# Kernel optimization log

Hardware: AMD Instinct MI355X
Metric: run time of the kernel (lower is better)

## Reference

```python
import jax, jax.numpy as jnp
import numpy as np

N, E = 50000, 800000
D_IN, D_HID, D_OUT, K = 128, 64, 64, 3
SLOPE = 0.2


def _xavier(key, shape):
    fan_out, fan_in = shape[0], shape[-1]
    if len(shape) == 3:  # att param (1, heads, 2*out)
        fan_out, fan_in = shape[1], shape[2]
    a = jnp.sqrt(6.0 / (fan_in + fan_out)).astype(jnp.float32)
    return jax.random.uniform(key, shape, jnp.float32, -a, a)


def setup_inputs() -> dict:
    key = jax.random.key(0)
    ks = jax.random.split(key, 9)
    x = jax.random.normal(ks[0], (N, D_IN), jnp.float32)
    edge_index = jax.random.randint(ks[1], (2, E), 0, N, jnp.int64)
    return {
        "x": x,
        "edge_index": edge_index,
        "W1": _xavier(ks[2], (D_HID, D_IN)),        # lin weight layer 1
        "att1": _xavier(ks[3], (1, 1, 2 * D_HID)),
        "bias1": jnp.zeros((D_HID,), jnp.float32),
        "resW1": _xavier(ks[4], (D_HID, D_IN)),     # res_fc (128 != 64)
        "W2": _xavier(ks[5], (D_OUT, D_HID)),       # lin weight layer 2
        "att2": _xavier(ks[6], (1, 1, 2 * D_OUT)),
        "bias2": jnp.zeros((D_OUT,), jnp.float32),
    }


def _agdn_conv(x, src, dst, W, att, bias, resW, heads):
    n = x.shape[0]
    h0 = (x @ W.T).reshape(n, heads, -1)                      # [N, h, out]
    feats = [h0]
    f = h0
    for _ in range(K):  # K-hop scatter-add propagation
        f = jax.ops.segment_sum(f[src], dst, num_segments=n)  # [N, h, out]
        feats.append(f)
    stack = jnp.stack(feats, axis=2)                          # [N, h, K+1, out]
    cat = jnp.concatenate(
        [jnp.broadcast_to(h0[:, :, None, :], stack.shape), stack], axis=-1
    )                                                         # [N, h, K+1, 2*out]
    score = jax.nn.leaky_relu((cat * att).sum(-1), SLOPE)     # [N, h, K+1]
    attn = jax.nn.softmax(score, axis=2)[..., None]
    out = (stack * attn).sum(axis=2).reshape(n, -1)           # [N, h*out]
    res = (x @ resW.T) if resW is not None else h0.reshape(n, -1)
    return out + res + bias


def reference(x, edge_index, W1, att1, bias1, resW1, W2, att2, bias2):
    src, dst = edge_index[0], edge_index[1]
    h = _agdn_conv(x, src, dst, W1, att1, bias1, resW1, heads=1)
    h = jax.nn.elu(h)  # eval mode: dropout is identity
    out = _agdn_conv(h, src, dst, W2, att2, bias2, None, heads=1)
    return out
```

## Files before the change

kernel.cpp:

```cpp
#include <hip/hip_runtime.h>
#include <math.h>


#define EPB 4096
#define CAP 8192

typedef __attribute__((ext_vector_type(8))) short bf16x8;
typedef __attribute__((ext_vector_type(4))) float f32x4;
typedef __attribute__((ext_vector_type(2))) float f32x2;

__device__ __forceinline__ float bf2f(unsigned short u)
{
    unsigned int t = ((unsigned int)u) << 16;
    return __builtin_bit_cast(float, t);
}
__device__ __forceinline__ unsigned short f2bf(float f)
{
    unsigned int t = __builtin_bit_cast(unsigned int, f);
    t += 0x7FFFu + ((t >> 16) & 1u);
    return (unsigned short)(t >> 16);
}
__device__ __forceinline__ float bflo(unsigned int u)
{
    return __builtin_bit_cast(float, u << 16);
}
__device__ __forceinline__ float bfhi(unsigned int u)
{
    return __builtin_bit_cast(float, u & 0xFFFF0000u);
}
__device__ __forceinline__ f32x2 up2v(unsigned int u)
{
    f32x2 r;
    r.x = bflo(u);
    r.y = bfhi(u);
    return r;
}

__global__ __launch_bounds__(256)
void convert_w_kernel(const float* __restrict__ W1, const float* __restrict__ Wres,
                      const float* __restrict__ W2,
                      unsigned short* __restrict__ w1b, unsigned short* __restrict__ w2b)
{
    int i = blockIdx.x * 256 + threadIdx.x;
    if (i < 8192)       w1b[i] = f2bf(W1[i]);
    else if (i < 16384) w1b[i] = f2bf(Wres[i - 8192]);
    else if (i < 20480) w2b[i - 16384] = f2bf(W2[i - 16384]);
}

#define LD1 136
__global__ __launch_bounds__(256)
void gemm_l1_mfma(const float* __restrict__ x,
                  const unsigned short* __restrict__ w1b,
                  unsigned short* __restrict__ h0, float* __restrict__ res, int n)
{
    __shared__ unsigned short xs[64 * LD1];
    __shared__ unsigned short ws[128 * LD1];
    const int tid = threadIdx.x;
    const int n0 = blockIdx.x * 64;

    for (int i = tid; i < 128 * 16; i += 256) {
        int r = i >> 4, c8 = (i & 15) * 8;
        *(uint4*)&ws[r * LD1 + c8] = *(const uint4*)&w1b[r * 128 + c8];
    }
    for (int i = tid; i < 64 * 32; i += 256) {
        int r = i >> 5, c4 = (i & 31) * 4;
        int nn = n0 + r;
        float4 v = (nn < n) ? *(const float4*)&x[(size_t)nn * 128 + c4]
                            : make_float4(0.f, 0.f, 0.f, 0.f);
        uint2 o;
        o.x = (unsigned)f2bf(v.x) | ((unsigned)f2bf(v.y) << 16);
        o.y = (unsigned)f2bf(v.z) | ((unsigned)f2bf(v.w) << 16);
        *(uint2*)&xs[r * LD1 + c4] = o;
    }
    __syncthreads();

    const int wv = tid >> 6, l = tid & 63;
    const int lrow = l & 15, lk = l >> 4;
    f32x4 acc[8] = {};
    const unsigned short* ax = &xs[(wv * 16 + lrow) * LD1 + lk * 8];
    const unsigned short* bw = &ws[lrow * LD1 + lk * 8];

    #pragma unroll
    for (int s = 0; s < 4; ++s) {
        bf16x8 a = *(const bf16x8*)&ax[s * 32];
        #pragma unroll
        for (int t = 0; t < 8; ++t) {
            bf16x8 b = *(const bf16x8*)&bw[(size_t)t * 16 * LD1 + s * 32];
            acc[t] = __builtin_amdgcn_mfma_f32_16x16x32_bf16(a, b, acc[t], 0, 0, 0);
        }
    }

    #pragma unroll
    for (int t = 0; t < 8; ++t) {
        #pragma unroll
        for (int r = 0; r < 4; ++r) {
            int node = n0 + wv * 16 + lk * 4 + r;
            if (node < n) {
                if (t < 4) h0[(size_t)node * 64 + t * 16 + lrow] = f2bf(acc[t][r]);
                else       res[(size_t)node * 64 + (t - 4) * 16 + lrow] = acc[t][r];
            }
        }
    }
}

#define LD2 72
__global__ __launch_bounds__(256)
void gemm_l2_mfma(const float* __restrict__ h,
                  const unsigned short* __restrict__ w2b,
                  unsigned short* __restrict__ h0, int n)
{
    __shared__ unsigned short xs[64 * LD2];
    __shared__ unsigned short ws[64 * LD2];
    const int tid = threadIdx.x;
    const int n0 = blockIdx.x * 64;

    for (int i = tid; i < 64 * 8; i += 256) {
        int r = i >> 3, c8 = (i & 7) * 8;
        *(uint4*)&ws[r * LD2 + c8] = *(const uint4*)&w2b[r * 64 + c8];
    }
    for (int i = tid; i < 64 * 16; i += 256) {
        int r = i >> 4, c4 = (i & 15) * 4;
        int nn = n0 + r;
        float4 v = (nn < n) ? *(const float4*)&h[(size_t)nn * 64 + c4]
                            : make_float4(0.f, 0.f, 0.f, 0.f);
        uint2 o;
        o.x = (unsigned)f2bf(v.x) | ((unsigned)f2bf(v.y) << 16);
        o.y = (unsigned)f2bf(v.z) | ((unsigned)f2bf(v.w) << 16);
        *(uint2*)&xs[r * LD2 + c4] = o;
    }
    __syncthreads();

    const int wv = tid >> 6, l = tid & 63;
    const int lrow = l & 15, lk = l >> 4;
    f32x4 acc[4] = {};
    const unsigned short* ax = &xs[(wv * 16 + lrow) * LD2 + lk * 8];
    const unsigned short* bw = &ws[lrow * LD2 + lk * 8];

    #pragma unroll
    for (int s = 0; s < 2; ++s) {
        bf16x8 a = *(const bf16x8*)&ax[s * 32];
        #pragma unroll
        for (int t = 0; t < 4; ++t) {
            bf16x8 b = *(const bf16x8*)&bw[(size_t)t * 16 * LD2 + s * 32];
            acc[t] = __builtin_amdgcn_mfma_f32_16x16x32_bf16(a, b, acc[t], 0, 0, 0);
        }
    }

    #pragma unroll
    for (int t = 0; t < 4; ++t) {
        #pragma unroll
        for (int r = 0; r < 4; ++r) {
            int node = n0 + wv * 16 + lk * 4 + r;
            if (node < n)
                h0[(size_t)node * 64 + t * 16 + lrow] = f2bf(acc[t][r]);
        }
    }
}

__global__ __launch_bounds__(256)
void part_hist_kernel(const int* __restrict__ dst, int* __restrict__ table,
                      int E, int NB)
{
    __shared__ int h[256];
    h[threadIdx.x] = 0;
    __syncthreads();
    int base = blockIdx.x * EPB;
    for (int i = threadIdx.x; i < EPB; i += 256) {
        int e = base + i;
        if (e < E) atomicAdd(&h[((unsigned)dst[e]) >> 8], 1);
    }
    __syncthreads();
    table[threadIdx.x * NB + blockIdx.x] = h[threadIdx.x];
}

__global__ __launch_bounds__(256)
void scanA_kernel(const int* __restrict__ cnt, int* __restrict__ excl,
                  int* __restrict__ bsum, int n)
{
    __shared__ int sh[256];
    int i = blockIdx.x * 256 + threadIdx.x;
    int v = (i < n) ? cnt[i] : 0;
    sh[threadIdx.x] = v;
    __syncthreads();
    #pragma unroll
    for (int off = 1; off < 256; off <<= 1) {
        int t = (threadIdx.x >= off) ? sh[threadIdx.x - off] : 0;
        __syncthreads();
        sh[threadIdx.x] += t;
        __syncthreads();
    }
    if (i < n) excl[i] = sh[threadIdx.x] - v;
    if (threadIdx.x == 255) bsum[blockIdx.x] = sh[255];
}

__global__ __launch_bounds__(256)
void scanB_kernel(const int* __restrict__ bsum, int* __restrict__ bofs, int nb)
{
    __shared__ int sh[256];
    int v = (threadIdx.x < nb) ? bsum[threadIdx.x] : 0;
    sh[threadIdx.x] = v;
    __syncthreads();
    #pragma unroll
    for (int off = 1; off < 256; off <<= 1) {
        int t = (threadIdx.x >= off) ? sh[threadIdx.x - off] : 0;
        __syncthreads();
        sh[threadIdx.x] += t;
        __syncthreads();
    }
    if (threadIdx.x < nb) bofs[threadIdx.x] = sh[threadIdx.x] - v;
}

__global__ __launch_bounds__(256)
void part_scatter_kernel(const int* __restrict__ src, const int* __restrict__ dst,
                         const int* __restrict__ exclT, const int* __restrict__ bofsT,
                         unsigned int* __restrict__ packed, int E, int NB)
{
    __shared__ int lhist[256];
    __shared__ int sh[256];
    __shared__ int lexcl[256];
    __shared__ int lcur[256];
    __shared__ int gb2[256];
    __shared__ unsigned int lp[EPB];
    __shared__ unsigned char lbin[EPB];

    const int tid = threadIdx.x;
    const int base = blockIdx.x * EPB;
    const int cntE = min(EPB, E - base);

    unsigned int pv[16];
    int pb[16];
    lhist[tid] = 0;
    __syncthreads();
    #pragma unroll
    for (int it = 0; it < 16; ++it) {
        int i = it * 256 + tid;
        pv[it] = 0; pb[it] = -1;
        if (i < cntE) {
            int e = base + i;
            unsigned int p = (((unsigned)dst[e]) << 16) | (unsigned)src[e];
            pv[it] = p;
            pb[it] = (int)(p >> 24);
            atomicAdd(&lhist[pb[it]], 1);
        }
    }
    __syncthreads();
    sh[tid] = lhist[tid];
    __syncthreads();
    #pragma unroll
    for (int off = 1; off < 256; off <<= 1) {
        int t = (tid >= off) ? sh[tid - off] : 0;
        __syncthreads();
        sh[tid] += t;
        __syncthreads();
    }
    lexcl[tid] = sh[tid] - lhist[tid];
    lcur[tid] = sh[tid] - lhist[tid];
    int ti = tid * NB + blockIdx.x;
    gb2[tid] = exclT[ti] + bofsT[ti >> 8] - lexcl[tid];
    __syncthreads();
    #pragma unroll
    for (int it = 0; it < 16; ++it) {
        if (pb[it] >= 0) {
            int slot = atomicAdd(&lcur[pb[it]], 1);
            lp[slot] = pv[it];
            lbin[slot] = (unsigned char)pb[it];
        }
    }
    __syncthreads();
    for (int i = tid; i < cntE; i += 256)
        packed[gb2[lbin[i]] + i] = lp[i];
}

__global__ __launch_bounds__(256)
void bucket_build_kernel(const unsigned int* __restrict__ packed,
                         const int* __restrict__ exclT, const int* __restrict__ bofsT,
                         int* __restrict__ rowptr, int* __restrict__ col,
                         int E, int NB, int N)
{
    __shared__ int h[256];
    __shared__ int sh[256];
    __shared__ int lcur[256];
    __shared__ int colL[CAP];

    const int b = blockIdx.x;
    const int t = threadIdx.x;
    int i0 = exclT[b * NB] + bofsT[(b * NB) >> 8];
    int bn = (b + 1) * NB;
    int i1 = exclT[bn] + bofsT[bn >> 8];

    h[t] = 0;
    __syncthreads();
    for (int i = i0 + t; i < i1; i += 256)
        atomicAdd(&h[(packed[i] >> 16) & 255], 1);
    __syncthreads();
    sh[t] = h[t];
    __syncthreads();
    #pragma unroll
    for (int off = 1; off < 256; off <<= 1) {
        int v = (t >= off) ? sh[t - off] : 0;
        __syncthreads();
        sh[t] += v;
        __syncthreads();
    }
    int excl = sh[t] - h[t];
    int d = b * 256 + t;
    if (d < N) rowptr[d] = i0 + excl;
    if (b == gridDim.x - 1 && t == 0) rowptr[N] = E;
    lcur[t] = excl;
    __syncthreads();
    for (int i = i0 + t; i < i1; i += 256) {
        unsigned int p = packed[i];
        int lo = (p >> 16) & 255;
        int s = (int)(p & 0xFFFFu);
        int r = atomicAdd(&lcur[lo], 1);
        if (r < CAP) colL[r] = s;
        else col[i0 + r] = s;
    }
    __syncthreads();
    int cB = i1 - i0;
    for (int i = t; i < cB && i < CAP; i += 256)
        col[i0 + i] = colL[i];
}

__global__ __launch_bounds__(256)
void hop_csr_kernel(const unsigned short* __restrict__ fin,
                    unsigned short* __restrict__ fout,
                    const int* __restrict__ rowptr, const int* __restrict__ col, int n)
{
    int node = blockIdx.x * 4 + (threadIdx.x >> 6);
    if (node >= n) return;
    int lane = threadIdx.x & 63;
    int sub = lane >> 3;
    int fo = (lane & 7) * 8;

    int beg = rowptr[node], end = rowptr[node + 1];
    int deg = end - beg;
    f32x2 ac[4] = {};
    for (int b = 0; b < deg; b += 16) {
        int e0 = beg + b + sub, e1 = e0 + 8;
        uint4 u0 = make_uint4(0, 0, 0, 0), u1 = make_uint4(0, 0, 0, 0);
        if (e0 < end) { int s = col[e0]; u0 = *(const uint4*)&fin[(size_t)s * 64 + fo]; }
        if (e1 < end) { int s = col[e1]; u1 = *(const uint4*)&fin[(size_t)s * 64 + fo]; }
        ac[0] += up2v(u0.x); ac[1] += up2v(u0.y);
        ac[2] += up2v(u0.z); ac[3] += up2v(u0.w);
        ac[0] += up2v(u1.x); ac[1] += up2v(u1.y);
        ac[2] += up2v(u1.z); ac[3] += up2v(u1.w);
    }
    float a[8] = {ac[0].x, ac[0].y, ac[1].x, ac[1].y,
                  ac[2].x, ac[2].y, ac[3].x, ac[3].y};
    #pragma unroll
    for (int off = 8; off <= 32; off <<= 1)
        #pragma unroll
        for (int k = 0; k < 8; ++k)
            a[k] += __shfl_xor(a[k], off);
    if (sub == 0) {
        uint4 o;
        o.x = (unsigned)f2bf(a[0]) | ((unsigned)f2bf(a[1]) << 16);
        o.y = (unsigned)f2bf(a[2]) | ((unsigned)f2bf(a[3]) << 16);
        o.z = (unsigned)f2bf(a[4]) | ((unsigned)f2bf(a[5]) << 16);
        o.w = (unsigned)f2bf(a[6]) | ((unsigned)f2bf(a[7]) << 16);
        *(uint4*)&fout[(size_t)node * 64 + fo] = o;
    }
}

template<int MODE>
__global__ __launch_bounds__(256)
void hop3_combine_kernel(const unsigned short* __restrict__ h0,
                         const unsigned short* __restrict__ f1,
                         const unsigned short* __restrict__ f2,
                         const float* __restrict__ res, const float* __restrict__ att,
                         const float* __restrict__ bias, float* __restrict__ out,
                         const int* __restrict__ rowptr, const int* __restrict__ col, int n)
{
    int node = blockIdx.x * 4 + (threadIdx.x >> 6);
    if (node >= n) return;
    int lane = threadIdx.x & 63;
    int sub = lane >> 3;
    int fo = (lane & 7) * 8;
    size_t rbase = (size_t)node * 64 + fo;

    int beg = rowptr[node], end = rowptr[node + 1];
    int deg = end - beg;
    f32x2 ac[4] = {};
    for (int b = 0; b < deg; b += 16) {
        int e0 = beg + b + sub, e1 = e0 + 8;
        uint4 u0 = make_uint4(0, 0, 0, 0), u1 = make_uint4(0, 0, 0, 0);
        if (e0 < end) { int s = col[e0]; u0 = *(const uint4*)&f2[(size_t)s * 64 + fo]; }
        if (e1 < end) { int s = col[e1]; u1 = *(const uint4*)&f2[(size_t)s * 64 + fo]; }
        ac[0] += up2v(u0.x); ac[1] += up2v(u0.y);
        ac[2] += up2v(u0.z); ac[3] += up2v(u0.w);
        ac[0] += up2v(u1.x); ac[1] += up2v(u1.y);
        ac[2] += up2v(u1.z); ac[3] += up2v(u1.w);
    }
    float a[8] = {ac[0].x, ac[0].y, ac[1].x, ac[1].y,
                  ac[2].x, ac[2].y, ac[3].x, ac[3].y};
    #pragma unroll
    for (int off = 8; off <= 32; off <<= 1)
        #pragma unroll
        for (int k = 0; k < 8; ++k)
            a[k] += __shfl_xor(a[k], off);

    uint4 r0 = *(const uint4*)&h0[rbase];
    uint4 r1 = *(const uint4*)&f1[rbase];
    uint4 r2 = *(const uint4*)&f2[rbase];
    float v0f[8] = {bflo(r0.x), bfhi(r0.x), bflo(r0.y), bfhi(r0.y),
                    bflo(r0.z), bfhi(r0.z), bflo(r0.w), bfhi(r0.w)};
    float v1f[8] = {bflo(r1.x), bfhi(r1.x), bflo(r1.y), bfhi(r1.y),
                    bflo(r1.z), bfhi(r1.z), bflo(r1.w), bfhi(r1.w)};
    float v2f[8] = {bflo(r2.x), bfhi(r2.x), bflo(r2.y), bfhi(r2.y),
                    bflo(r2.z), bfhi(r2.z), bflo(r2.w), bfhi(r2.w)};

    float4 alo0 = *(const float4*)&att[fo];
    float4 alo1 = *(const float4*)&att[fo + 4];
    float4 ahi0 = *(const float4*)&att[64 + fo];
    float4 ahi1 = *(const float4*)&att[64 + fo + 4];
    float alo[8] = {alo0.x, alo0.y, alo0.z, alo0.w, alo1.x, alo1.y, alo1.z, alo1.w};
    float ahi[8] = {ahi0.x, ahi0.y, ahi0.z, ahi0.w, ahi1.x, ahi1.y, ahi1.z, ahi1.w};

    float p0 = 0.f, q0 = 0.f, q1 = 0.f, q2 = 0.f, q3 = 0.f;
    #pragma unroll
    for (int j = 0; j < 8; ++j) {
        p0 += v0f[j] * alo[j];
        q0 += v0f[j] * ahi[j];
        q1 += v1f[j] * ahi[j];
        q2 += v2f[j] * ahi[j];
        q3 += a[j]   * ahi[j];
    }
    #pragma unroll
    for (int off = 1; off <= 4; off <<= 1) {
        p0 += __shfl_xor(p0, off);
        q0 += __shfl_xor(q0, off);
        q1 += __shfl_xor(q1, off);
        q2 += __shfl_xor(q2, off);
        q3 += __shfl_xor(q3, off);
    }

    float s0 = p0 + q0, s1 = p0 + q1, s2 = p0 + q2, s3 = p0 + q3;
    s0 = s0 > 0.f ? s0 : 0.2f * s0;
    s1 = s1 > 0.f ? s1 : 0.2f * s1;
    s2 = s2 > 0.f ? s2 : 0.2f * s2;
    s3 = s3 > 0.f ? s3 : 0.2f * s3;
    float m = fmaxf(fmaxf(s0, s1), fmaxf(s2, s3));
    float E0 = __expf(s0 - m), E1 = __expf(s1 - m);
    float E2 = __expf(s2 - m), E3 = __expf(s3 - m);
    float inv = 1.f / (E0 + E1 + E2 + E3);
    float w0 = E0 * inv, w1 = E1 * inv, w2 = E2 * inv, w3 = E3 * inv;

    float rsv[8];
    if (MODE == 0) {
        float4 ra = *(const float4*)&res[rbase];
        float4 rb = *(const float4*)&res[rbase + 4];
        rsv[0] = ra.x; rsv[1] = ra.y; rsv[2] = ra.z; rsv[3] = ra.w;
        rsv[4] = rb.x; rsv[5] = rb.y; rsv[6] = rb.z; rsv[7] = rb.w;
    } else {
        #pragma unroll
        for (int j = 0; j < 8; ++j) rsv[j] = v0f[j];
    }
    float4 ba = *(const float4*)&bias[fo];
    float4 bb = *(const float4*)&bias[fo + 4];
    float bi[8] = {ba.x, ba.y, ba.z, ba.w, bb.x, bb.y, bb.z, bb.w};

    float o[8];
    #pragma unroll
    for (int j = 0; j < 8; ++j) {
        float v = w0 * v0f[j] + w1 * v1f[j] + w2 * v2f[j] + w3 * a[j];
        v += rsv[j] + bi[j];
        if (MODE == 0) v = v > 0.f ? v : __expf(v) - 1.f;
        o[j] = v;
    }
    if (sub == 0) {
        *(float4*)&out[rbase]     = make_float4(o[0], o[1], o[2], o[3]);
        *(float4*)&out[rbase + 4] = make_float4(o[4], o[5], o[6], o[7]);
    }
}

extern "C" void kernel_launch(void* const* d_in, const int* in_sizes, int n_in,
                              void* d_out, int out_size, void* d_ws, size_t ws_size,
                              hipStream_t stream)
{
    const float* x     = (const float*)d_in[0];
    const int*   ei    = (const int*)  d_in[1];
    const float* W1    = (const float*)d_in[2];
    const float* att1  = (const float*)d_in[3];
    const float* bias1 = (const float*)d_in[4];
    const float* resW1 = (const float*)d_in[5];
    const float* W2    = (const float*)d_in[6];
    const float* att2  = (const float*)d_in[7];
    const float* bias2 = (const float*)d_in[8];

    const int N_ = in_sizes[0] / 128;
    const int E_ = in_sizes[1] / 2;
    const int* src = ei;
    const int* dst = ei + E_;

    float* out = (float*)d_out;
    size_t S = (size_t)N_ * 64;
    unsigned short* h0 = (unsigned short*)d_ws;
    unsigned short* f1 = h0 + S;
    unsigned short* f2 = f1 + S;
    int* rowptr = (int*)(f2 + S);
    int* col    = rowptr + (N_ + 1);

    const int NB    = (E_ + EPB - 1) / EPB;
    const int NBUCK = (N_ + 255) / 256;

    unsigned int* packed = (unsigned int*)f1;
    int* table = (int*)(col + E_);
    int* exclT = table + 256 * NB;
    int* bsumT = exclT + 256 * NB;
    int* bofsT = bsumT + 256;
    unsigned short* w1b = (unsigned short*)(bofsT + 256);
    unsigned short* w2b = w1b + 16384;

    dim3 blk(256);
    int grid_g    = (N_ + 63) / 64;
    int node_grid = (N_ + 3) / 4;
    int nT        = 256 * NB;
    int nbT       = (nT + 255) / 256;

    convert_w_kernel<<<80, blk, 0, stream>>>(W1, resW1, W2, w1b, w2b);
    part_hist_kernel<<<NB, blk, 0, stream>>>(dst, table, E_, NB);
    scanA_kernel<<<nbT, blk, 0, stream>>>(table, exclT, bsumT, nT);
    scanB_kernel<<<1, blk, 0, stream>>>(bsumT, bofsT, nbT);
    part_scatter_kernel<<<NB, blk, 0, stream>>>(src, dst, exclT, bofsT, packed, E_, NB);
    bucket_build_kernel<<<NBUCK, blk, 0, stream>>>(packed, exclT, bofsT, rowptr, col,
                                                   E_, NB, N_);

    gemm_l1_mfma<<<grid_g, blk, 0, stream>>>(x, w1b, h0, out, N_);
    hop_csr_kernel<<<node_grid, blk, 0, stream>>>(h0, f1, rowptr, col, N_);
    hop_csr_kernel<<<node_grid, blk, 0, stream>>>(f1, f2, rowptr, col, N_);
    hop3_combine_kernel<0><<<node_grid, blk, 0, stream>>>(h0, f1, f2, out, att1, bias1, out,
                                                          rowptr, col, N_);

    gemm_l2_mfma<<<grid_g, blk, 0, stream>>>(out, w2b, h0, N_);
    hop_csr_kernel<<<node_grid, blk, 0, stream>>>(h0, f1, rowptr, col, N_);
    hop_csr_kernel<<<node_grid, blk, 0, stream>>>(f1, f2, rowptr, col, N_);
    hop3_combine_kernel<1><<<node_grid, blk, 0, stream>>>(h0, f1, f2, nullptr, att2, bias2, out,
                                                          rowptr, col, N_);
}
```

Measured before the change: 212.5 us.

## Map two nodes per wavefront in hop kernels and stage buckets in LDS

The CSR hop and hop3-combine kernels now give each node 32 lanes instead of 64, so one wavefront handles two nodes. Each node walks its edges 8 at a time and needs one fewer shuffle-reduction step, which cuts idle lanes for average-degree nodes. The bucket build kernel caches the packed edge words in LDS and stores column indices as 16-bit values, so packed is read from global memory only once. The weight bf16 conversion is folded into the histogram kernel, removing one launch. The risk is that high-degree nodes now get half the lanes each.

```diff
diff --git a/kernel.cpp b/kernel.cpp
--- a/kernel.cpp
+++ b/kernel.cpp
@@ -9,11 +9,6 @@
 typedef __attribute__((ext_vector_type(4))) float f32x4;
 typedef __attribute__((ext_vector_type(2))) float f32x2;
 
-__device__ __forceinline__ float bf2f(unsigned short u)
-{
-    unsigned int t = ((unsigned int)u) << 16;
-    return __builtin_bit_cast(float, t);
-}
 __device__ __forceinline__ unsigned short f2bf(float f)
 {
     unsigned int t = __builtin_bit_cast(unsigned int, f);
@@ -34,17 +29,6 @@
     r.x = bflo(u);
     r.y = bfhi(u);
     return r;
-}
-
-__global__ __launch_bounds__(256)
-void convert_w_kernel(const float* __restrict__ W1, const float* __restrict__ Wres,
-                      const float* __restrict__ W2,
-                      unsigned short* __restrict__ w1b, unsigned short* __restrict__ w2b)
-{
-    int i = blockIdx.x * 256 + threadIdx.x;
-    if (i < 8192)       w1b[i] = f2bf(W1[i]);
-    else if (i < 16384) w1b[i] = f2bf(Wres[i - 8192]);
-    else if (i < 20480) w2b[i - 16384] = f2bf(W2[i - 16384]);
 }
 
 #define LD1 136
@@ -159,8 +143,16 @@
 
 __global__ __launch_bounds__(256)
 void part_hist_kernel(const int* __restrict__ dst, int* __restrict__ table,
-                      int E, int NB)
-{
+                      int E, int NB,
+                      const float* __restrict__ W1, const float* __restrict__ Wres,
+                      const float* __restrict__ W2,
+                      unsigned short* __restrict__ w1b, unsigned short* __restrict__ w2b)
+{
+    int gi = blockIdx.x * 256 + threadIdx.x;
+    if (gi < 8192)       w1b[gi] = f2bf(W1[gi]);
+    else if (gi < 16384) w1b[gi] = f2bf(Wres[gi - 8192]);
+    else if (gi < 20480) w2b[gi - 16384] = f2bf(W2[gi - 16384]);
+
     __shared__ int h[256];
     h[threadIdx.x] = 0;
     __syncthreads();
@@ -280,18 +272,23 @@
     __shared__ int h[256];
     __shared__ int sh[256];
     __shared__ int lcur[256];
-    __shared__ int colL[CAP];
+    __shared__ unsigned int lp[CAP];
+    __shared__ unsigned short colS[CAP];
 
     const int b = blockIdx.x;
     const int t = threadIdx.x;
     int i0 = exclT[b * NB] + bofsT[(b * NB) >> 8];
     int bn = (b + 1) * NB;
     int i1 = exclT[bn] + bofsT[bn >> 8];
+    int cB = i1 - i0;
 
     h[t] = 0;
     __syncthreads();
-    for (int i = i0 + t; i < i1; i += 256)
-        atomicAdd(&h[(packed[i] >> 16) & 255], 1);
+    for (int i = t; i < cB; i += 256) {
+        unsigned int p = packed[i0 + i];
+        if (i < CAP) lp[i] = p;
+        atomicAdd(&h[(p >> 16) & 255], 1);
+    }
     __syncthreads();
     sh[t] = h[t];
     __syncthreads();
@@ -308,18 +305,16 @@
     if (b == gridDim.x - 1 && t == 0) rowptr[N] = E;
     lcur[t] = excl;
     __syncthreads();
-    for (int i = i0 + t; i < i1; i += 256) {
-        unsigned int p = packed[i];
+    for (int i = t; i < cB; i += 256) {
+        unsigned int p = (i < CAP) ? lp[i] : packed[i0 + i];
         int lo = (p >> 16) & 255;
-        int s = (int)(p & 0xFFFFu);
         int r = atomicAdd(&lcur[lo], 1);
-        if (r < CAP) colL[r] = s;
-        else col[i0 + r] = s;
-    }
-    __syncthreads();
-    int cB = i1 - i0;
+        if (r < CAP) colS[r] = (unsigned short)(p & 0xFFFFu);
+        else col[i0 + r] = (int)(p & 0xFFFFu);
+    }
+    __syncthreads();
     for (int i = t; i < cB && i < CAP; i += 256)
-        col[i0 + i] = colL[i];
+        col[i0 + i] = (int)colS[i];
 }
 
 __global__ __launch_bounds__(256)
@@ -327,20 +322,20 @@
                     unsigned short* __restrict__ fout,
                     const int* __restrict__ rowptr, const int* __restrict__ col, int n)
 {
-    int node = blockIdx.x * 4 + (threadIdx.x >> 6);
+    int lane = threadIdx.x & 63;
+    int node = blockIdx.x * 8 + ((threadIdx.x >> 6) << 1) + (lane >> 5);
     if (node >= n) return;
-    int lane = threadIdx.x & 63;
-    int sub = lane >> 3;
+    int sub = (lane >> 3) & 3;
     int fo = (lane & 7) * 8;
 
     int beg = rowptr[node], end = rowptr[node + 1];
-    int deg = end - beg;
     f32x2 ac[4] = {};
-    for (int b = 0; b < deg; b += 16) {
-        int e0 = beg + b + sub, e1 = e0 + 8;
-        uint4 u0 = make_uint4(0, 0, 0, 0), u1 = make_uint4(0, 0, 0, 0);
-        if (e0 < end) { int s = col[e0]; u0 = *(const uint4*)&fin[(size_t)s * 64 + fo]; }
-        if (e1 < end) { int s = col[e1]; u1 = *(const uint4*)&fin[(size_t)s * 64 + fo]; }
+    for (int b = beg + sub; b < end; b += 8) {
+        int s0 = col[b];
+        uint4 u0 = *(const uint4*)&fin[(size_t)s0 * 64 + fo];
+        uint4 u1 = make_uint4(0, 0, 0, 0);
+        int e1 = b + 4;
+        if (e1 < end) { int s1 = col[e1]; u1 = *(const uint4*)&fin[(size_t)s1 * 64 + fo]; }
         ac[0] += up2v(u0.x); ac[1] += up2v(u0.y);
         ac[2] += up2v(u0.z); ac[3] += up2v(u0.w);
         ac[0] += up2v(u1.x); ac[1] += up2v(u1.y);
@@ -349,7 +344,7 @@
     float a[8] = {ac[0].x, ac[0].y, ac[1].x, ac[1].y,
                   ac[2].x, ac[2].y, ac[3].x, ac[3].y};
     #pragma unroll
-    for (int off = 8; off <= 32; off <<= 1)
+    for (int off = 8; off <= 16; off <<= 1)
         #pragma unroll
         for (int k = 0; k < 8; ++k)
             a[k] += __shfl_xor(a[k], off);
@@ -372,21 +367,21 @@
                          const float* __restrict__ bias, float* __restrict__ out,
                          const int* __restrict__ rowptr, const int* __restrict__ col, int n)
 {
-    int node = blockIdx.x * 4 + (threadIdx.x >> 6);
+    int lane = threadIdx.x & 63;
+    int node = blockIdx.x * 8 + ((threadIdx.x >> 6) << 1) + (lane >> 5);
     if (node >= n) return;
-    int lane = threadIdx.x & 63;
-    int sub = lane >> 3;
+    int sub = (lane >> 3) & 3;
     int fo = (lane & 7) * 8;
     size_t rbase = (size_t)node * 64 + fo;
 
     int beg = rowptr[node], end = rowptr[node + 1];
-    int deg = end - beg;
     f32x2 ac[4] = {};
-    for (int b = 0; b < deg; b += 16) {
-        int e0 = beg + b + sub, e1 = e0 + 8;
-        uint4 u0 = make_uint4(0, 0, 0, 0), u1 = make_uint4(0, 0, 0, 0);
-        if (e0 < end) { int s = col[e0]; u0 = *(const uint4*)&f2[(size_t)s * 64 + fo]; }
-        if (e1 < end) { int s = col[e1]; u1 = *(const uint4*)&f2[(size_t)s * 64 + fo]; }
+    for (int b = beg + sub; b < end; b += 8) {
+        int s0 = col[b];
+        uint4 u0 = *(const uint4*)&f2[(size_t)s0 * 64 + fo];
+        uint4 u1 = make_uint4(0, 0, 0, 0);
+        int e1 = b + 4;
+        if (e1 < end) { int s1 = col[e1]; u1 = *(const uint4*)&f2[(size_t)s1 * 64 + fo]; }
         ac[0] += up2v(u0.x); ac[1] += up2v(u0.y);
         ac[2] += up2v(u0.z); ac[3] += up2v(u0.w);
         ac[0] += up2v(u1.x); ac[1] += up2v(u1.y);
@@ -395,7 +390,7 @@
     float a[8] = {ac[0].x, ac[0].y, ac[1].x, ac[1].y,
                   ac[2].x, ac[2].y, ac[3].x, ac[3].y};
     #pragma unroll
-    for (int off = 8; off <= 32; off <<= 1)
+    for (int off = 8; off <= 16; off <<= 1)
         #pragma unroll
         for (int k = 0; k < 8; ++k)
             a[k] += __shfl_xor(a[k], off);
@@ -514,12 +509,12 @@
 
     dim3 blk(256);
     int grid_g    = (N_ + 63) / 64;
-    int node_grid = (N_ + 3) / 4;
+    int node_grid = (N_ + 7) / 8;
     int nT        = 256 * NB;
     int nbT       = (nT + 255) / 256;
 
-    convert_w_kernel<<<80, blk, 0, stream>>>(W1, resW1, W2, w1b, w2b);
-    part_hist_kernel<<<NB, blk, 0, stream>>>(dst, table, E_, NB);
+    part_hist_kernel<<<NB, blk, 0, stream>>>(dst, table, E_, NB,
+                                             W1, resW1, W2, w1b, w2b);
     scanA_kernel<<<nbT, blk, 0, stream>>>(table, exclT, bsumT, nT);
     scanB_kernel<<<1, blk, 0, stream>>>(bsumT, bofsT, nbT);
     part_scatter_kernel<<<NB, blk, 0, stream>>>(src, dst, exclT, bofsT, packed, E_, NB);
```

Result: faster. 179.7 us (-15.4%).
